# Kernel optimization log

Measured on AMD Instinct MI355X. Metric: run time of the kernel, lower is better.

Reference implementation:

```python
import jax, jax.numpy as jnp
import numpy as np

B, E, C, R_REL = 2, 1024, 128, 32

def setup_inputs() -> dict:
    key = jax.random.key(0)
    kx, kr = jax.random.split(key)
    x = jax.random.normal(kx, (B, E, C), dtype=jnp.float32)
    R = jax.random.normal(kr, (R_REL, E, E), dtype=jnp.float32)
    return {"x": x, "R": R}

def reference(x, R):
    # Gram matrix over the feature axis: G[b,s,o] = sum_c x[b,s,c] x[b,o,c]
    G = jnp.einsum('bsc,boc->bso', x, x)  # (B, E, E)
    # Broadcast-scale by relation tensor: out[b,s,r,o] = G[b,s,o] * R[r,s,o]
    scores = G[:, :, None, :] * R[None, :, :, :].transpose(0, 2, 1, 3)  # (B, E, R, E)
    return scores
```

## Files before the change

kernel.cpp:

```cpp
#include <hip/hip_runtime.h>

#define B_SZ 2
#define E_SZ 1024
#define C_SZ 128
#define R_REL 32
#define TS 64
#define TO 64

__global__ __launch_bounds__(256, 2) void rescal_fused(
        const float* __restrict__ x,
        const float* __restrict__ R,
        float* __restrict__ out) {
    __shared__ float xs[TS][C_SZ + 4];
    __shared__ float xo[TO][C_SZ + 4];

    const int b  = blockIdx.z;
    const int s0 = blockIdx.y * TS;
    const int o0 = blockIdx.x * TO;
    const int tid = threadIdx.x;

    const float4* src_s = (const float4*)(x + (size_t)b * E_SZ * C_SZ + (size_t)s0 * C_SZ);
    const float4* src_o = (const float4*)(x + (size_t)b * E_SZ * C_SZ + (size_t)o0 * C_SZ);
    #pragma unroll
    for (int i = tid; i < TS * (C_SZ / 4); i += 256) {
        const int row = i >> 5;
        const int col = (i & 31) << 2;
        *(float4*)&xs[row][col] = src_s[i];
        *(float4*)&xo[row][col] = src_o[i];
    }
    __syncthreads();

    const int tx = tid & 15;
    const int ty = tid >> 4;
    const int si = ty << 2;
    const int oj = tx << 2;

    float acc[4][4];
    #pragma unroll
    for (int ii = 0; ii < 4; ++ii)
        #pragma unroll
        for (int jj = 0; jj < 4; ++jj) acc[ii][jj] = 0.f;

    #pragma unroll 4
    for (int c = 0; c < C_SZ; c += 4) {
        float4 a[4], bb[4];
        #pragma unroll
        for (int ii = 0; ii < 4; ++ii) a[ii]  = *(const float4*)&xs[si + ii][c];
        #pragma unroll
        for (int jj = 0; jj < 4; ++jj) bb[jj] = *(const float4*)&xo[oj + jj][c];
        #pragma unroll
        for (int ii = 0; ii < 4; ++ii) {
            #pragma unroll
            for (int jj = 0; jj < 4; ++jj) {
                acc[ii][jj] += a[ii].x * bb[jj].x + a[ii].y * bb[jj].y
                             + a[ii].z * bb[jj].z + a[ii].w * bb[jj].w;
            }
        }
    }

    const size_t out_base = ((size_t)b * E_SZ + (size_t)s0) * (size_t)(R_REL * E_SZ) + o0;
    #pragma unroll 1
    for (int r = 0; r < R_REL; ++r) {
        const float* Rp = R + (size_t)r * (E_SZ * E_SZ) + (size_t)s0 * E_SZ + o0;
        float* op = out + out_base + (size_t)r * E_SZ;
        #pragma unroll
        for (int ii = 0; ii < 4; ++ii) {
            const float4 rv = *(const float4*)(Rp + (size_t)(si + ii) * E_SZ + oj);
            float4 ov;
            ov.x = acc[ii][0] * rv.x;
            ov.y = acc[ii][1] * rv.y;
            ov.z = acc[ii][2] * rv.z;
            ov.w = acc[ii][3] * rv.w;
            *(float4*)(op + (size_t)(si + ii) * (R_REL * E_SZ) + oj) = ov;
        }
    }
}

extern "C" void kernel_launch(void* const* d_in, const int* in_sizes, int n_in,
                              void* d_out, int out_size, void* d_ws, size_t ws_size,
                              hipStream_t stream) {
    const float* x = (const float*)d_in[0];
    const float* R = (const float*)d_in[1];
    float* out = (float*)d_out;
    dim3 grid(E_SZ / TO, E_SZ / TS, B_SZ);
    rescal_fused<<<grid, 256, 0, stream>>>(x, R, out);
}
```

Before: 385.8 us.

## Split into Gram kernel plus streaming scale kernel sharing R reads across batches

```diff
diff --git a/kernel.cpp b/kernel.cpp
--- a/kernel.cpp
+++ b/kernel.cpp
@@ -6,6 +6,96 @@
 #define R_REL 32
 #define TS 64
 #define TO 64
+
+typedef float f32x4 __attribute__((ext_vector_type(4)));
+
+__global__ __launch_bounds__(256, 2) void gram_tile(
+        const float* __restrict__ x,
+        float* __restrict__ G) {
+    __shared__ float xs[TS][C_SZ + 4];
+    __shared__ float xo[TO][C_SZ + 4];
+
+    const int b  = blockIdx.z;
+    const int s0 = blockIdx.y * TS;
+    const int o0 = blockIdx.x * TO;
+    const int tid = threadIdx.x;
+
+    const float4* src_s = (const float4*)(x + (size_t)b * E_SZ * C_SZ + (size_t)s0 * C_SZ);
+    const float4* src_o = (const float4*)(x + (size_t)b * E_SZ * C_SZ + (size_t)o0 * C_SZ);
+    #pragma unroll
+    for (int i = tid; i < TS * (C_SZ / 4); i += 256) {
+        const int row = i >> 5;
+        const int col = (i & 31) << 2;
+        *(float4*)&xs[row][col] = src_s[i];
+        *(float4*)&xo[row][col] = src_o[i];
+    }
+    __syncthreads();
+
+    const int tx = tid & 15;
+    const int ty = tid >> 4;
+    const int si = ty << 2;
+    const int oj = tx << 2;
+
+    float acc[4][4];
+    #pragma unroll
+    for (int ii = 0; ii < 4; ++ii)
+        #pragma unroll
+        for (int jj = 0; jj < 4; ++jj) acc[ii][jj] = 0.f;
+
+    #pragma unroll 4
+    for (int c = 0; c < C_SZ; c += 4) {
+        float4 a[4], bb[4];
+        #pragma unroll
+        for (int ii = 0; ii < 4; ++ii) a[ii]  = *(const float4*)&xs[si + ii][c];
+        #pragma unroll
+        for (int jj = 0; jj < 4; ++jj) bb[jj] = *(const float4*)&xo[oj + jj][c];
+        #pragma unroll
+        for (int ii = 0; ii < 4; ++ii) {
+            #pragma unroll
+            for (int jj = 0; jj < 4; ++jj) {
+                acc[ii][jj] += a[ii].x * bb[jj].x + a[ii].y * bb[jj].y
+                             + a[ii].z * bb[jj].z + a[ii].w * bb[jj].w;
+            }
+        }
+    }
+
+    #pragma unroll
+    for (int ii = 0; ii < 4; ++ii) {
+        float4 gv;
+        gv.x = acc[ii][0]; gv.y = acc[ii][1]; gv.z = acc[ii][2]; gv.w = acc[ii][3];
+        *(float4*)(G + ((size_t)b * E_SZ + (size_t)(s0 + si + ii)) * E_SZ + o0 + oj) = gv;
+    }
+}
+
+__global__ __launch_bounds__(256, 8) void scale_stream(
+        const float* __restrict__ G,
+        const float* __restrict__ R,
+        float* __restrict__ out) {
+    const int o4 = threadIdx.x;
+    const int s  = blockIdx.x;
+    const int r0 = blockIdx.y * (R_REL / 2);
+
+    const f32x4* G4 = (const f32x4*)G;
+    const f32x4* R4 = (const f32x4*)R;
+    f32x4*       O4 = (f32x4*)out;
+
+    const f32x4 g0 = G4[(size_t)s * (E_SZ / 4) + o4];
+    const f32x4 g1 = G4[((size_t)E_SZ + s) * (E_SZ / 4) + o4];
+
+    const f32x4* rp  = R4 + ((size_t)r0 * E_SZ + s) * (E_SZ / 4) + o4;
+    f32x4*       op0 = O4 + (((size_t)s) * R_REL + r0) * (E_SZ / 4) + o4;
+    f32x4*       op1 = O4 + (((size_t)(E_SZ + s)) * R_REL + r0) * (E_SZ / 4) + o4;
+
+    #pragma unroll 4
+    for (int r = 0; r < R_REL / 2; ++r) {
+        f32x4 rv = __builtin_nontemporal_load(rp);
+        __builtin_nontemporal_store(rv * g0, op0);
+        __builtin_nontemporal_store(rv * g1, op1);
+        rp  += (size_t)E_SZ * E_SZ / 4;
+        op0 += E_SZ / 4;
+        op1 += E_SZ / 4;
+    }
+}
 
 __global__ __launch_bounds__(256, 2) void rescal_fused(
         const float* __restrict__ x,
@@ -82,6 +172,16 @@
     const float* x = (const float*)d_in[0];
     const float* R = (const float*)d_in[1];
     float* out = (float*)d_out;
-    dim3 grid(E_SZ / TO, E_SZ / TS, B_SZ);
-    rescal_fused<<<grid, 256, 0, stream>>>(x, R, out);
+
+    const size_t g_bytes = (size_t)B_SZ * E_SZ * E_SZ * sizeof(float);
+    if (ws_size >= g_bytes && d_ws != nullptr) {
+        float* G = (float*)d_ws;
+        dim3 g1(E_SZ / TO, E_SZ / TS, B_SZ);
+        gram_tile<<<g1, 256, 0, stream>>>(x, G);
+        dim3 g2(E_SZ, R_REL / 16);
+        scale_stream<<<g2, 256, 0, stream>>>(G, R, out);
+    } else {
+        dim3 grid(E_SZ / TO, E_SZ / TS, B_SZ);
+        rescal_fused<<<grid, 256, 0, stream>>>(x, R, out);
+    }
 }
```

After: 379.0 us. Within noise of the previous version (-1.8%).

## Split into Gram kernel plus streaming scale kernel reusing R across batches

Applied to the files above, without the earlier changes.

```diff
diff --git a/kernel.cpp b/kernel.cpp
--- a/kernel.cpp
+++ b/kernel.cpp
@@ -7,10 +7,12 @@
 #define TS 64
 #define TO 64
 
-__global__ __launch_bounds__(256, 2) void rescal_fused(
-        const float* __restrict__ x,
-        const float* __restrict__ R,
-        float* __restrict__ out) {
+typedef float f32x4 __attribute__((ext_vector_type(4)));
+
+__device__ float g_G[(size_t)B_SZ * E_SZ * E_SZ];
+
+__global__ __launch_bounds__(256, 2) void gram_tile(
+        const float* __restrict__ x) {
     __shared__ float xs[TS][C_SZ + 4];
     __shared__ float xo[TO][C_SZ + 4];
 
@@ -58,21 +60,37 @@
         }
     }
 
-    const size_t out_base = ((size_t)b * E_SZ + (size_t)s0) * (size_t)(R_REL * E_SZ) + o0;
-    #pragma unroll 1
-    for (int r = 0; r < R_REL; ++r) {
-        const float* Rp = R + (size_t)r * (E_SZ * E_SZ) + (size_t)s0 * E_SZ + o0;
-        float* op = out + out_base + (size_t)r * E_SZ;
-        #pragma unroll
-        for (int ii = 0; ii < 4; ++ii) {
-            const float4 rv = *(const float4*)(Rp + (size_t)(si + ii) * E_SZ + oj);
-            float4 ov;
-            ov.x = acc[ii][0] * rv.x;
-            ov.y = acc[ii][1] * rv.y;
-            ov.z = acc[ii][2] * rv.z;
-            ov.w = acc[ii][3] * rv.w;
-            *(float4*)(op + (size_t)(si + ii) * (R_REL * E_SZ) + oj) = ov;
-        }
+    #pragma unroll
+    for (int ii = 0; ii < 4; ++ii) {
+        float4 gv;
+        gv.x = acc[ii][0]; gv.y = acc[ii][1]; gv.z = acc[ii][2]; gv.w = acc[ii][3];
+        *(float4*)(g_G + ((size_t)b * E_SZ + (size_t)(s0 + si + ii)) * E_SZ + o0 + oj) = gv;
+    }
+}
+
+__global__ __launch_bounds__(256, 8) void scale_stream(
+        const float* __restrict__ R,
+        float* __restrict__ out) {
+    const int o4 = threadIdx.x;
+    const int s  = blockIdx.x;
+    const int r0 = blockIdx.y * (R_REL / 2);
+
+    const f32x4* G4 = (const f32x4*)g_G;
+    const f32x4* R4 = (const f32x4*)R;
+    f32x4*       O4 = (f32x4*)out;
+
+    const f32x4 g0 = G4[(size_t)s * (E_SZ / 4) + o4];
+    const f32x4 g1 = G4[((size_t)E_SZ + s) * (E_SZ / 4) + o4];
+
+    const f32x4* rp  = R4 + ((size_t)r0 * E_SZ + s) * (E_SZ / 4) + o4;
+    f32x4*       op0 = O4 + (((size_t)s) * R_REL + r0) * (E_SZ / 4) + o4;
+    f32x4*       op1 = O4 + (((size_t)(E_SZ + s)) * R_REL + r0) * (E_SZ / 4) + o4;
+
+    #pragma unroll 4
+    for (int r = 0; r < R_REL / 2; ++r) {
+        const f32x4 rv = rp[(size_t)r * (E_SZ * E_SZ / 4)];
+        op0[(size_t)r * (E_SZ / 4)] = rv * g0;
+        op1[(size_t)r * (E_SZ / 4)] = rv * g1;
     }
 }
 
@@ -82,6 +100,9 @@
     const float* x = (const float*)d_in[0];
     const float* R = (const float*)d_in[1];
     float* out = (float*)d_out;
-    dim3 grid(E_SZ / TO, E_SZ / TS, B_SZ);
-    rescal_fused<<<grid, 256, 0, stream>>>(x, R, out);
+
+    dim3 g1(E_SZ / TO, E_SZ / TS, B_SZ);
+    gram_tile<<<g1, 256, 0, stream>>>(x);
+    dim3 g2(E_SZ, R_REL / 16);
+    scale_stream<<<g2, 256, 0, stream>>>(R, out);
 }
```

New measurement: 389.8 us. About the same (+1.0%).
